# Performance work log

Hardware: AMD Instinct MI355X
Metric: run time of the kernel (lower is better)

## Reference

```python
import jax, jax.numpy as jnp
import numpy as np

B, T, C, H = 4, 2048, 1024, 16
D = C // H  # head_size = 64


def setup_inputs() -> dict:
    key = jax.random.key(0)
    k1, k2, k3 = jax.random.split(key, 3)
    x = jax.random.normal(k1, (B, T, C), dtype=jnp.float32)
    w_qkv = jax.random.normal(k2, (C, 3 * C), dtype=jnp.float32) * (C ** -0.5)
    b_qkv = jnp.zeros((3 * C,), dtype=jnp.float32)
    w_proj = jax.random.normal(k3, (C, C), dtype=jnp.float32) * (C ** -0.5)
    b_proj = jnp.zeros((C,), dtype=jnp.float32)
    return {"x": x, "w_qkv": w_qkv, "b_qkv": b_qkv, "w_proj": w_proj, "b_proj": b_proj}


def reference(x, w_qkv, b_qkv, w_proj, b_proj):
    b, t, c = x.shape
    qkv = x @ w_qkv + b_qkv                      # [B,T,3C]
    q, k, v = jnp.split(qkv, 3, axis=-1)
    # [B,T,C] -> [B,H,T,D]
    q = q.reshape(b, t, H, D).transpose(0, 2, 1, 3)
    k = k.reshape(b, t, H, D).transpose(0, 2, 1, 3)
    v = v.reshape(b, t, H, D).transpose(0, 2, 1, 3)
    attn = jnp.einsum('bhqd,bhkd->bhqk', q, k) * (D ** -0.5)
    causal = jnp.tril(jnp.ones((t, t), dtype=bool))
    attn = jnp.where(causal[None, None], attn, -jnp.inf)
    attn = jax.nn.softmax(attn, axis=-1)
    # dropout: eval mode (identity)
    out = jnp.einsum('bhqk,bhkd->bhqd', attn, v)
    out = out.transpose(0, 2, 1, 3).reshape(b, t, c)
    return out @ w_proj + b_proj
```

## Files before the change

kernel.cpp:

```cpp
#include <hip/hip_runtime.h>

#define B_ 4
#define T_ 2048
#define C_ 1024
#define H_ 16
#define D_ 64

typedef __attribute__((ext_vector_type(8))) short short8;
typedef __attribute__((ext_vector_type(4))) float f32x4;

__device__ inline unsigned short f2bf(float f) {
    union { float f; unsigned u; } v; v.f = f;
    unsigned r = v.u + 0x7fffu + ((v.u >> 16) & 1u);
    return (unsigned short)(r >> 16);
}

__device__ inline unsigned int pk_bf16(float a, float b) {
#if __has_builtin(__builtin_amdgcn_cvt_pk_bf16_f32)
    typedef __attribute__((ext_vector_type(2))) __bf16 bf16x2;
    bf16x2 v = __builtin_amdgcn_cvt_pk_bf16_f32(a, b);
    return __builtin_bit_cast(unsigned int, v);
#else
    return (unsigned)f2bf(a) | ((unsigned)f2bf(b) << 16);
#endif
}

__device__ inline void async_ld16(const void* g, void* lds) {
    __builtin_amdgcn_global_load_lds(
        (const __attribute__((address_space(1))) unsigned int*)g,
        (__attribute__((address_space(3))) unsigned int*)lds, 16, 0, 0);
}

#define MFMA_BF16 __builtin_amdgcn_mfma_f32_16x16x32_bf16

__global__ __launch_bounds__(256) void prep_all(
    const float* __restrict__ x, const float* __restrict__ w_qkv,
    const float* __restrict__ w_proj,
    unsigned short* __restrict__ xb, unsigned short* __restrict__ wqkvT,
    unsigned short* __restrict__ wprojT)
{
    const int bid = blockIdx.x;
    if (bid < 8192) {
        int i = (bid * 256 + threadIdx.x) * 4;
        float4 v = *(const float4*)(x + i);
        uint2 o;
        o.x = pk_bf16(v.x, v.y);
        o.y = pk_bf16(v.z, v.w);
        *(uint2*)(xb + i) = o;
        return;
    }
    __shared__ float tile[32][33];
    const int tt = bid - 8192;
    int bx = tt & 127;
    const int by = tt >> 7;
    const float* src; unsigned short* dst; int Cc;
    if (bx < 96) { src = w_qkv;  dst = wqkvT;  Cc = 3072; }
    else         { src = w_proj; dst = wprojT; Cc = 1024; bx -= 96; }
    const int tx = threadIdx.x & 31, ty = threadIdx.x >> 5;
    #pragma unroll
    for (int r = 0; r < 32; r += 8)
        tile[ty + r][tx] = src[(size_t)(by*32 + ty + r) * Cc + bx*32 + tx];
    __syncthreads();
    #pragma unroll
    for (int r = 0; r < 32; r += 8)
        dst[(size_t)(bx*32 + ty + r) * 1024 + by*32 + tx] = f2bf(tile[tx][ty + r]);
}

__global__ __launch_bounds__(256) void gemm_qkv(
    const unsigned short* __restrict__ A,
    const unsigned short* __restrict__ BT,
    const float* __restrict__ bias,
    unsigned short* __restrict__ qb, unsigned short* __restrict__ kb,
    unsigned short* __restrict__ vtb)
{
    __shared__ unsigned short As[2][128 * 64];
    __shared__ unsigned short Bs[2][128 * 64];
    const int tid = threadIdx.x;
    const int wave = tid >> 6, lane = tid & 63;
    const int wm = wave >> 1, wn = wave & 1;
    const int l15 = lane & 15, lq = lane >> 4;
    const int bid = blockIdx.x;
    const int xcd = bid & 7, idx = bid >> 3;
    const int m0 = (xcd * 8 + (idx & 7)) * 128;
    const int n0 = (idx >> 3) * 128;
    const int sel = n0 >> 10;
    const int row8 = lane >> 3;
    const int chx8 = ((lane & 7) ^ row8) * 8;
    const int cxa = l15 & 7;

    f32x4 acc[4][4] = {};

#define STAGE(buf, K0) do { _Pragma("unroll") \
    for (int c = 0; c < 4; ++c) { \
        const int r = wave*32 + c*8; \
        async_ld16(A  + (size_t)(m0 + r + row8)*1024 + (K0) + chx8, \
                   (char*)&As[buf][0] + r*128); \
        async_ld16(BT + (size_t)(n0 + r + row8)*1024 + (K0) + chx8, \
                   (char*)&Bs[buf][0] + r*128); \
    } } while (0)

    STAGE(0, 0);
    __syncthreads();

    for (int t = 0; t < 16; ++t) {
        const int cur = t & 1;
        if (t < 15) STAGE(cur ^ 1, (t + 1) << 6);
        const unsigned short* Ac = &As[cur][0];
        const unsigned short* Bc = &Bs[cur][0];
        #pragma unroll
        for (int ks = 0; ks < 2; ++ks) {
            short8 af[4], bf[4];
            #pragma unroll
            for (int i = 0; i < 4; ++i) {
                const int ra = wm*64 + i*16 + l15;
                const int rb = wn*64 + i*16 + l15;
                af[i] = *(const short8*)&Ac[ra*64 + (((ks*4 + lq) ^ cxa) << 3)];
                bf[i] = *(const short8*)&Bc[rb*64 + (((ks*4 + lq) ^ cxa) << 3)];
            }
            if (sel < 2) {
                #pragma unroll
                for (int mi = 0; mi < 4; ++mi)
                    #pragma unroll
                    for (int ni = 0; ni < 4; ++ni)
                        acc[mi][ni] = MFMA_BF16(bf[ni], af[mi], acc[mi][ni], 0, 0, 0);
            } else {
                #pragma unroll
                for (int mi = 0; mi < 4; ++mi)
                    #pragma unroll
                    for (int ni = 0; ni < 4; ++ni)
                        acc[mi][ni] = MFMA_BF16(af[mi], bf[ni], acc[mi][ni], 0, 0, 0);
            }
        }
        __syncthreads();
    }
#undef STAGE

    if (sel < 2) {
        const float qs = (sel == 0) ? 0.180336880f : 1.0f;
        unsigned short* dst = (sel == 0) ? qb : kb;
        #pragma unroll
        for (int mi = 0; mi < 4; ++mi) {
            const int t = m0 + wm*64 + mi*16 + l15;
            const int bb = t >> 11, tt = t & 2047;
            #pragma unroll
            for (int ni = 0; ni < 4; ++ni) {
                const int nb = n0 + wn*64 + ni*16 + lq*4;
                const int hh = (nb >> 6) & 15, d0 = nb & 63;
                float4 bv = *(const float4*)(bias + nb);
                float v0 = (acc[mi][ni][0] + bv.x) * qs;
                float v1 = (acc[mi][ni][1] + bv.y) * qs;
                float v2 = (acc[mi][ni][2] + bv.z) * qs;
                float v3 = (acc[mi][ni][3] + bv.w) * qs;
                uint2 pk; pk.x = pk_bf16(v0, v1); pk.y = pk_bf16(v2, v3);
                *(uint2*)(dst + ((size_t)(bb*16 + hh)*2048 + tt)*64 + d0) = pk;
            }
        }
    } else {
        #pragma unroll
        for (int mi = 0; mi < 4; ++mi) {
            const int t0 = m0 + wm*64 + mi*16 + lq*4;
            const int bb = t0 >> 11, tt = t0 & 2047;
            const int tl = tt & 63;
            const int tp = (tt & ~63) | (tl & 32) | ((tl & 12) << 1) | ((tl & 16) >> 2);
            #pragma unroll
            for (int ni = 0; ni < 4; ++ni) {
                const int n = n0 + wn*64 + ni*16 + l15;
                const int hh = (n >> 6) & 15, d = n & 63;
                const float bs = bias[n];
                uint2 pk;
                pk.x = pk_bf16(acc[mi][ni][0] + bs, acc[mi][ni][1] + bs);
                pk.y = pk_bf16(acc[mi][ni][2] + bs, acc[mi][ni][3] + bs);
                *(uint2*)(vtb + ((size_t)(bb*16 + hh)*64 + d)*2048 + tp) = pk;
            }
        }
    }
}

__global__ __launch_bounds__(256) void gemm_proj(
    const unsigned short* __restrict__ A,
    const unsigned short* __restrict__ BT,
    const float* __restrict__ bias,
    float* __restrict__ out)
{
    __shared__ unsigned short As[2][128 * 64];
    __shared__ unsigned short Bs[2][128 * 64];
    const int tid = threadIdx.x;
    const int wave = tid >> 6, lane = tid & 63;
    const int wm = wave >> 1, wn = wave & 1;
    const int l15 = lane & 15, lq = lane >> 4;
    const int bid = blockIdx.x;
    const int xcd = bid & 7, idx = bid >> 3;
    const int m0 = (xcd * 8 + (idx & 7)) * 128;
    const int n0 = (idx >> 3) * 128;
    const int row8 = lane >> 3;
    const int chx8 = ((lane & 7) ^ row8) * 8;
    const int cxa = l15 & 7;

    f32x4 acc[4][4] = {};

#define PSTAGE(buf, K0) do { _Pragma("unroll") \
    for (int c = 0; c < 4; ++c) { \
        const int r = wave*32 + c*8; \
        async_ld16(A  + (size_t)(m0 + r + row8)*1024 + (K0) + chx8, \
                   (char*)&As[buf][0] + r*128); \
        async_ld16(BT + (size_t)(n0 + r + row8)*1024 + (K0) + chx8, \
                   (char*)&Bs[buf][0] + r*128); \
    } } while (0)

    PSTAGE(0, 0);
    __syncthreads();

    for (int t = 0; t < 16; ++t) {
        const int cur = t & 1;
        if (t < 15) PSTAGE(cur ^ 1, (t + 1) << 6);
        const unsigned short* Ac = &As[cur][0];
        const unsigned short* Bc = &Bs[cur][0];
        #pragma unroll
        for (int ks = 0; ks < 2; ++ks) {
            short8 af[4], bf[4];
            #pragma unroll
            for (int i = 0; i < 4; ++i) {
                const int ra = wm*64 + i*16 + l15;
                const int rb = wn*64 + i*16 + l15;
                af[i] = *(const short8*)&Ac[ra*64 + (((ks*4 + lq) ^ cxa) << 3)];
                bf[i] = *(const short8*)&Bc[rb*64 + (((ks*4 + lq) ^ cxa) << 3)];
            }
            #pragma unroll
            for (int mi = 0; mi < 4; ++mi)
                #pragma unroll
                for (int ni = 0; ni < 4; ++ni)
                    acc[mi][ni] = MFMA_BF16(bf[ni], af[mi], acc[mi][ni], 0, 0, 0);
        }
        __syncthreads();
    }
#undef PSTAGE

    #pragma unroll
    for (int mi = 0; mi < 4; ++mi) {
        const int m = m0 + wm*64 + mi*16 + l15;
        #pragma unroll
        for (int ni = 0; ni < 4; ++ni) {
            const int nb = n0 + wn*64 + ni*16 + lq*4;
            float4 bv = *(const float4*)(bias + nb);
            float4 o;
            o.x = acc[mi][ni][0] + bv.x;
            o.y = acc[mi][ni][1] + bv.y;
            o.z = acc[mi][ni][2] + bv.z;
            o.w = acc[mi][ni][3] + bv.w;
            *(float4*)(out + (size_t)m * 1024 + nb) = o;
        }
    }
}

__global__ __launch_bounds__(256, 2) void attn_mfma(
    const unsigned short* __restrict__ qb,
    const unsigned short* __restrict__ kb,
    const unsigned short* __restrict__ vtb,
    unsigned short* __restrict__ ab)
{
    extern __shared__ unsigned char smem[];
    const int tid  = threadIdx.x;
    const int wave = tid >> 6, lane = tid & 63;
    const int l15  = lane & 15, lq = lane >> 4;
    const int linear = blockIdx.x;
    const int xc  = linear & 7;
    const int idx = linear >> 3;
    const int bh  = xc * 8 + (idx & 7);
    const int qblk = 31 - (idx >> 3);
    const int q0 = qblk * 64;
    const int b = bh >> 4, h = bh & 15;
    const size_t base = (size_t)bh * 2048 * 64;

    unsigned short* Kw = (unsigned short*)(smem + wave * 16384);
    unsigned short* Vw = Kw + 4096;

    const int row8 = lane >> 3;
    const int chx8 = ((lane & 7) ^ row8) * 8;

#define STAGE_K(J0) do { _Pragma("unroll") for (int op = 0; op < 8; ++op) \
    async_ld16(kb + base + (size_t)((J0) + op*8 + row8)*64 + chx8, \
               (char*)Kw + op*1024); } while (0)
#define STAGE_V(J0) do { _Pragma("unroll") for (int op = 0; op < 8; ++op) \
    async_ld16(vtb + base + (size_t)(op*8 + row8)*2048 + (J0) + chx8, \
               (char*)Vw + op*1024); } while (0)

    short8 qf[2][4];
    #pragma unroll
    for (int ks = 0; ks < 2; ++ks)
        #pragma unroll
        for (int nq = 0; nq < 4; ++nq)
            qf[ks][nq] = *(const short8*)(qb + base
                + (size_t)(q0 + nq*16 + l15)*64 + ks*32 + lq*8);

    f32x4 o[4][4] = {};
    float lacc[4] = {0.f, 0.f, 0.f, 0.f};

    const int jfirst = wave * 64;
    const int nt = (qblk >= wave) ? ((qblk - wave) >> 2) + 1 : 0;

    if (nt > 0) { STAGE_K(jfirst); STAGE_V(jfirst); }

    for (int i = 0; i < nt; ++i) {
        const int j0 = jfirst + i * 256;
        const bool more = (i + 1 < nt);

        asm volatile("s_waitcnt vmcnt(8)" ::: "memory");

        short8 kf0[4], kf1[4];
        #pragma unroll
        for (int ni = 0; ni < 4; ++ni) {
            const unsigned short* kr = Kw + (ni*16 + l15) * 64;
            kf0[ni] = *(const short8*)(kr + (((0*4 + lq) ^ (l15 & 7)) << 3));
            kf1[ni] = *(const short8*)(kr + (((1*4 + lq) ^ (l15 & 7)) << 3));
        }
        f32x4 s[4][4] = {};
        #pragma unroll
        for (int ni = 0; ni < 4; ++ni)
            #pragma unroll
            for (int nq = 0; nq < 4; ++nq) {
                s[ni][nq] = MFMA_BF16(kf0[ni], qf[0][nq], s[ni][nq], 0, 0, 0);
                s[ni][nq] = MFMA_BF16(kf1[ni], qf[1][nq], s[ni][nq], 0, 0, 0);
            }
        asm volatile("s_waitcnt lgkmcnt(0)" ::: "memory");
        if (more) STAGE_K(j0 + 256);

        if (j0 == q0) {
            #pragma unroll
            for (int ni = 0; ni < 4; ++ni)
                #pragma unroll
                for (int nq = 0; nq < 4; ++nq)
                    #pragma unroll
                    for (int r = 0; r < 4; ++r)
                        if (ni*16 + lq*4 + r > nq*16 + l15)
                            s[ni][nq][r] = -1e30f;
        }

        short8 pf[2][4];
        #pragma unroll
        for (int c = 0; c < 2; ++c)
            #pragma unroll
            for (int nq = 0; nq < 4; ++nq) {
                float p0 = __builtin_amdgcn_exp2f(s[2*c  ][nq][0]);
                float p1 = __builtin_amdgcn_exp2f(s[2*c  ][nq][1]);
                float p2 = __builtin_amdgcn_exp2f(s[2*c  ][nq][2]);
                float p3 = __builtin_amdgcn_exp2f(s[2*c  ][nq][3]);
                float p4 = __builtin_amdgcn_exp2f(s[2*c+1][nq][0]);
                float p5 = __builtin_amdgcn_exp2f(s[2*c+1][nq][1]);
                float p6 = __builtin_amdgcn_exp2f(s[2*c+1][nq][2]);
                float p7 = __builtin_amdgcn_exp2f(s[2*c+1][nq][3]);
                lacc[nq] += ((p0 + p1) + (p2 + p3)) + ((p4 + p5) + (p6 + p7));
                uint4 pu;
                pu.x = pk_bf16(p0, p1); pu.y = pk_bf16(p2, p3);
                pu.z = pk_bf16(p4, p5); pu.w = pk_bf16(p6, p7);
                pf[c][nq] = __builtin_bit_cast(short8, pu);
            }

        if (more) asm volatile("s_waitcnt vmcnt(8)" ::: "memory");
        else      asm volatile("s_waitcnt vmcnt(0)" ::: "memory");

        #pragma unroll
        for (int c = 0; c < 2; ++c) {
            short8 vf[4];
            #pragma unroll
            for (int nd = 0; nd < 4; ++nd)
                vf[nd] = *(const short8*)(Vw + (nd*16 + l15) * 64
                    + (((c*4 + lq) ^ (l15 & 7)) << 3));
            #pragma unroll
            for (int nq = 0; nq < 4; ++nq)
                #pragma unroll
                for (int nd = 0; nd < 4; ++nd)
                    o[nq][nd] = MFMA_BF16(pf[c][nq], vf[nd], o[nq][nd], 0, 0, 0);
        }
        asm volatile("s_waitcnt lgkmcnt(0)" ::: "memory");
        if (more) STAGE_V(j0 + 256);
    }
#undef STAGE_K
#undef STAGE_V

    #pragma unroll
    for (int nq = 0; nq < 4; ++nq) {
        float t = lacc[nq];
        t += __shfl_xor(t, 16);
        t += __shfl_xor(t, 32);
        if (lq == 0) ((float*)Kw)[nq*16 + l15] = t;
    }
    __syncthreads();
    const int qg = wave, d = lane;
    f32x4 linv4[4];
    #pragma unroll
    for (int j = 0; j < 4; ++j) {
        f32x4 lsum = {};
        #pragma unroll
        for (int w2 = 0; w2 < 4; ++w2)
            lsum += *(const f32x4*)((const float*)(smem + w2*16384) + qg*16 + j*4);
        #pragma unroll
        for (int r = 0; r < 4; ++r)
            linv4[j][r] = __builtin_amdgcn_rcpf(lsum[r]);
    }
    __syncthreads();
    #pragma unroll
    for (int nq = 0; nq < 4; ++nq)
        #pragma unroll
        for (int nd = 0; nd < 4; ++nd) {
            const int row = nd*16 + l15;
            const int col = (nq*16 + lq*4 + 4*l15) & 63;
            *(f32x4*)((float*)Kw + row*64 + col) = o[nq][nd];
        }
    __syncthreads();
    #pragma unroll
    for (int j = 0; j < 4; ++j) {
        const int colb = (qg*16 + j*4 + 4*(d & 15)) & 63;
        f32x4 acc = {};
        #pragma unroll
        for (int w2 = 0; w2 < 4; ++w2)
            acc += *(const f32x4*)((const float*)(smem + w2*16384) + d*64 + colb);
        #pragma unroll
        for (int r = 0; r < 4; ++r) {
            const int q = qg*16 + j*4 + r;
            ab[(size_t)(b*2048 + q0 + q)*1024 + h*64 + d] = f2bf(acc[r] * linv4[j][r]);
        }
    }
}

extern "C" void kernel_launch(void* const* d_in, const int* in_sizes, int n_in,
                              void* d_out, int out_size, void* d_ws, size_t ws_size,
                              hipStream_t stream) {
    const float* x      = (const float*)d_in[0];
    const float* w_qkv  = (const float*)d_in[1];
    const float* b_qkv  = (const float*)d_in[2];
    const float* w_proj = (const float*)d_in[3];
    const float* b_proj = (const float*)d_in[4];
    float* out = (float*)d_out;

    unsigned short* xb     = (unsigned short*)d_ws;
    unsigned short* wqkvT  = xb + 8388608;
    unsigned short* wprojT = wqkvT + 3145728;
    unsigned short* qbuf   = wprojT + 1048576;
    unsigned short* kbuf   = qbuf + 8388608;
    unsigned short* vtbuf  = kbuf + 8388608;
    unsigned short* abuf   = vtbuf + 8388608;

    prep_all<<<12288, 256, 0, stream>>>(x, w_qkv, w_proj, xb, wqkvT, wprojT);
    gemm_qkv<<<1536, 256, 0, stream>>>(xb, wqkvT, b_qkv, qbuf, kbuf, vtbuf);
    attn_mfma<<<2048, 256, 65536, stream>>>(qbuf, kbuf, vtbuf, abuf);
    gemm_proj<<<512, 256, 0, stream>>>(abuf, wprojT, b_proj, out);
}
```

Baseline: 237.7 us.

## Halve GEMM K-tile to 32, raise occupancy, and hand-schedule async-load pipeline

Both GEMM kernels (QKV and output projection) now stage 32-wide K slices instead of 64, which halves LDS per block, and request 3 blocks per CU through launch bounds. The loop now uses explicit vmcnt/lgkmcnt waits, raw s_barrier, sched_barrier fences and setprio around the MFMA block, with a new swizzle for the smaller tile. The aim is more resident blocks and better overlap of global loads with MFMA work. In exchange it doubles the number of barriers per K step, and the register cap from the occupancy hint may cause spills.

```diff
diff --git a/kernel.cpp b/kernel.cpp
--- a/kernel.cpp
+++ b/kernel.cpp
@@ -66,15 +66,15 @@
         dst[(size_t)(bx*32 + ty + r) * 1024 + by*32 + tx] = f2bf(tile[tx][ty + r]);
 }
 
-__global__ __launch_bounds__(256) void gemm_qkv(
+__global__ __launch_bounds__(256, 3) void gemm_qkv(
     const unsigned short* __restrict__ A,
     const unsigned short* __restrict__ BT,
     const float* __restrict__ bias,
     unsigned short* __restrict__ qb, unsigned short* __restrict__ kb,
     unsigned short* __restrict__ vtb)
 {
-    __shared__ unsigned short As[2][128 * 64];
-    __shared__ unsigned short Bs[2][128 * 64];
+    __shared__ unsigned short As[2][128 * 32];
+    __shared__ unsigned short Bs[2][128 * 32];
     const int tid = threadIdx.x;
     const int wave = tid >> 6, lane = tid & 63;
     const int wm = wave >> 1, wn = wave & 1;
@@ -84,54 +84,61 @@
     const int m0 = (xcd * 8 + (idx & 7)) * 128;
     const int n0 = (idx >> 3) * 128;
     const int sel = n0 >> 10;
-    const int row8 = lane >> 3;
-    const int chx8 = ((lane & 7) ^ row8) * 8;
-    const int cxa = l15 & 7;
+    const int srow4 = lane >> 2;
+    const int schx  = ((lane & 3) ^ ((lane >> 3) & 3)) * 8;
+    const int rdch = ((lq ^ ((l15 >> 1) & 3)) << 4);
 
     f32x4 acc[4][4] = {};
 
 #define STAGE(buf, K0) do { _Pragma("unroll") \
-    for (int c = 0; c < 4; ++c) { \
-        const int r = wave*32 + c*8; \
-        async_ld16(A  + (size_t)(m0 + r + row8)*1024 + (K0) + chx8, \
-                   (char*)&As[buf][0] + r*128); \
-        async_ld16(BT + (size_t)(n0 + r + row8)*1024 + (K0) + chx8, \
-                   (char*)&Bs[buf][0] + r*128); \
+    for (int c = 0; c < 2; ++c) { \
+        const int R0 = (wave*2 + c) * 16; \
+        async_ld16(A  + (size_t)(m0 + R0 + srow4)*1024 + (K0) + schx, \
+                   (char*)&As[buf][0] + R0*64); \
+        async_ld16(BT + (size_t)(n0 + R0 + srow4)*1024 + (K0) + schx, \
+                   (char*)&Bs[buf][0] + R0*64); \
     } } while (0)
 
     STAGE(0, 0);
-    __syncthreads();
-
-    for (int t = 0; t < 16; ++t) {
+
+    #pragma unroll 2
+    for (int t = 0; t < 32; ++t) {
         const int cur = t & 1;
-        if (t < 15) STAGE(cur ^ 1, (t + 1) << 6);
-        const unsigned short* Ac = &As[cur][0];
-        const unsigned short* Bc = &Bs[cur][0];
-        #pragma unroll
-        for (int ks = 0; ks < 2; ++ks) {
-            short8 af[4], bf[4];
-            #pragma unroll
-            for (int i = 0; i < 4; ++i) {
-                const int ra = wm*64 + i*16 + l15;
-                const int rb = wn*64 + i*16 + l15;
-                af[i] = *(const short8*)&Ac[ra*64 + (((ks*4 + lq) ^ cxa) << 3)];
-                bf[i] = *(const short8*)&Bc[rb*64 + (((ks*4 + lq) ^ cxa) << 3)];
-            }
-            if (sel < 2) {
+        if (t < 31) {
+            STAGE(cur ^ 1, (t + 1) << 5);
+            asm volatile("s_waitcnt vmcnt(4)" ::: "memory");
+        } else {
+            asm volatile("s_waitcnt vmcnt(0)" ::: "memory");
+        }
+        __builtin_amdgcn_s_barrier();
+        __builtin_amdgcn_sched_barrier(0);
+        short8 af[4], bf[4];
+        #pragma unroll
+        for (int i = 0; i < 4; ++i) {
+            af[i] = *(const short8*)((const char*)&As[cur][0]
+                        + (wm*64 + i*16 + l15)*64 + rdch);
+            bf[i] = *(const short8*)((const char*)&Bs[cur][0]
+                        + (wn*64 + i*16 + l15)*64 + rdch);
+        }
+        asm volatile("s_waitcnt lgkmcnt(0)" ::: "memory");
+        __builtin_amdgcn_sched_barrier(0);
+        __builtin_amdgcn_s_setprio(1);
+        if (sel < 2) {
+            #pragma unroll
+            for (int mi = 0; mi < 4; ++mi)
                 #pragma unroll
-                for (int mi = 0; mi < 4; ++mi)
-                    #pragma unroll
-                    for (int ni = 0; ni < 4; ++ni)
-                        acc[mi][ni] = MFMA_BF16(bf[ni], af[mi], acc[mi][ni], 0, 0, 0);
-            } else {
+                for (int ni = 0; ni < 4; ++ni)
+                    acc[mi][ni] = MFMA_BF16(bf[ni], af[mi], acc[mi][ni], 0, 0, 0);
+        } else {
+            #pragma unroll
+            for (int mi = 0; mi < 4; ++mi)
                 #pragma unroll
-                for (int mi = 0; mi < 4; ++mi)
-                    #pragma unroll
-                    for (int ni = 0; ni < 4; ++ni)
-                        acc[mi][ni] = MFMA_BF16(af[mi], bf[ni], acc[mi][ni], 0, 0, 0);
-            }
-        }
-        __syncthreads();
+                for (int ni = 0; ni < 4; ++ni)
+                    acc[mi][ni] = MFMA_BF16(af[mi], bf[ni], acc[mi][ni], 0, 0, 0);
+        }
+        __builtin_amdgcn_s_setprio(0);
+        __builtin_amdgcn_s_barrier();
+        __builtin_amdgcn_sched_barrier(0);
     }
 #undef STAGE
 
@@ -176,14 +183,14 @@
     }
 }
 
-__global__ __launch_bounds__(256) void gemm_proj(
+__global__ __launch_bounds__(256, 3) void gemm_proj(
     const unsigned short* __restrict__ A,
     const unsigned short* __restrict__ BT,
     const float* __restrict__ bias,
     float* __restrict__ out)
 {
-    __shared__ unsigned short As[2][128 * 64];
-    __shared__ unsigned short Bs[2][128 * 64];
+    __shared__ unsigned short As[2][128 * 32];
+    __shared__ unsigned short Bs[2][128 * 32];
     const int tid = threadIdx.x;
     const int wave = tid >> 6, lane = tid & 63;
     const int wm = wave >> 1, wn = wave & 1;
@@ -192,46 +199,53 @@
     const int xcd = bid & 7, idx = bid >> 3;
     const int m0 = (xcd * 8 + (idx & 7)) * 128;
     const int n0 = (idx >> 3) * 128;
-    const int row8 = lane >> 3;
-    const int chx8 = ((lane & 7) ^ row8) * 8;
-    const int cxa = l15 & 7;
+    const int srow4 = lane >> 2;
+    const int schx  = ((lane & 3) ^ ((lane >> 3) & 3)) * 8;
+    const int rdch = ((lq ^ ((l15 >> 1) & 3)) << 4);
 
     f32x4 acc[4][4] = {};
 
 #define PSTAGE(buf, K0) do { _Pragma("unroll") \
-    for (int c = 0; c < 4; ++c) { \
-        const int r = wave*32 + c*8; \
-        async_ld16(A  + (size_t)(m0 + r + row8)*1024 + (K0) + chx8, \
-                   (char*)&As[buf][0] + r*128); \
-        async_ld16(BT + (size_t)(n0 + r + row8)*1024 + (K0) + chx8, \
-                   (char*)&Bs[buf][0] + r*128); \
+    for (int c = 0; c < 2; ++c) { \
+        const int R0 = (wave*2 + c) * 16; \
+        async_ld16(A  + (size_t)(m0 + R0 + srow4)*1024 + (K0) + schx, \
+                   (char*)&As[buf][0] + R0*64); \
+        async_ld16(BT + (size_t)(n0 + R0 + srow4)*1024 + (K0) + schx, \
+                   (char*)&Bs[buf][0] + R0*64); \
     } } while (0)
 
     PSTAGE(0, 0);
-    __syncthreads();
-
-    for (int t = 0; t < 16; ++t) {
+
+    #pragma unroll 2
+    for (int t = 0; t < 32; ++t) {
         const int cur = t & 1;
-        if (t < 15) PSTAGE(cur ^ 1, (t + 1) << 6);
-        const unsigned short* Ac = &As[cur][0];
-        const unsigned short* Bc = &Bs[cur][0];
-        #pragma unroll
-        for (int ks = 0; ks < 2; ++ks) {
-            short8 af[4], bf[4];
-            #pragma unroll
-            for (int i = 0; i < 4; ++i) {
-                const int ra = wm*64 + i*16 + l15;
-                const int rb = wn*64 + i*16 + l15;
-                af[i] = *(const short8*)&Ac[ra*64 + (((ks*4 + lq) ^ cxa) << 3)];
-                bf[i] = *(const short8*)&Bc[rb*64 + (((ks*4 + lq) ^ cxa) << 3)];
-            }
-            #pragma unroll
-            for (int mi = 0; mi < 4; ++mi)
-                #pragma unroll
-                for (int ni = 0; ni < 4; ++ni)
-                    acc[mi][ni] = MFMA_BF16(bf[ni], af[mi], acc[mi][ni], 0, 0, 0);
-        }
-        __syncthreads();
+        if (t < 31) {
+            PSTAGE(cur ^ 1, (t + 1) << 5);
+            asm volatile("s_waitcnt vmcnt(4)" ::: "memory");
+        } else {
+            asm volatile("s_waitcnt vmcnt(0)" ::: "memory");
+        }
+        __builtin_amdgcn_s_barrier();
+        __builtin_amdgcn_sched_barrier(0);
+        short8 af[4], bf[4];
+        #pragma unroll
+        for (int i = 0; i < 4; ++i) {
+            af[i] = *(const short8*)((const char*)&As[cur][0]
+                        + (wm*64 + i*16 + l15)*64 + rdch);
+            bf[i] = *(const short8*)((const char*)&Bs[cur][0]
+                        + (wn*64 + i*16 + l15)*64 + rdch);
+        }
+        asm volatile("s_waitcnt lgkmcnt(0)" ::: "memory");
+        __builtin_amdgcn_sched_barrier(0);
+        __builtin_amdgcn_s_setprio(1);
+        #pragma unroll
+        for (int mi = 0; mi < 4; ++mi)
+            #pragma unroll
+            for (int ni = 0; ni < 4; ++ni)
+                acc[mi][ni] = MFMA_BF16(bf[ni], af[mi], acc[mi][ni], 0, 0, 0);
+        __builtin_amdgcn_s_setprio(0);
+        __builtin_amdgcn_s_barrier();
+        __builtin_amdgcn_sched_barrier(0);
     }
 #undef PSTAGE
 
```

After: 325.6 us. 1.37x slower.

## Enlarge QKV GEMM tile to 256x128 and drop LDS double buffering

Applied to the files above, without the earlier changes.

The QKV projection GEMM now computes a 256x128 output tile per block instead of 128x128, so each wave holds 8x4 accumulator fragments and B-tile data is reused across twice as many rows. The grid is halved to 768 blocks. The double-buffered async prefetch is replaced by a single buffer with load, sync, compute, sync per K step, which keeps the LDS footprint the same but removes the overlap of global loads with MFMA work. Register pressure rises with the doubled accumulator count, which can lower occupancy.

```diff
diff --git a/kernel.cpp b/kernel.cpp
--- a/kernel.cpp
+++ b/kernel.cpp
@@ -73,59 +73,57 @@
     unsigned short* __restrict__ qb, unsigned short* __restrict__ kb,
     unsigned short* __restrict__ vtb)
 {
-    __shared__ unsigned short As[2][128 * 64];
-    __shared__ unsigned short Bs[2][128 * 64];
+    __shared__ unsigned short As[256 * 64];
+    __shared__ unsigned short Bs[128 * 64];
     const int tid = threadIdx.x;
     const int wave = tid >> 6, lane = tid & 63;
     const int wm = wave >> 1, wn = wave & 1;
     const int l15 = lane & 15, lq = lane >> 4;
     const int bid = blockIdx.x;
     const int xcd = bid & 7, idx = bid >> 3;
-    const int m0 = (xcd * 8 + (idx & 7)) * 128;
-    const int n0 = (idx >> 3) * 128;
+    const int m0 = (xcd * 4 + (idx & 3)) * 256;
+    const int n0 = (idx >> 2) * 128;
     const int sel = n0 >> 10;
     const int row8 = lane >> 3;
     const int chx8 = ((lane & 7) ^ row8) * 8;
     const int cxa = l15 & 7;
 
-    f32x4 acc[4][4] = {};
-
-#define STAGE(buf, K0) do { _Pragma("unroll") \
-    for (int c = 0; c < 4; ++c) { \
-        const int r = wave*32 + c*8; \
-        async_ld16(A  + (size_t)(m0 + r + row8)*1024 + (K0) + chx8, \
-                   (char*)&As[buf][0] + r*128); \
-        async_ld16(BT + (size_t)(n0 + r + row8)*1024 + (K0) + chx8, \
-                   (char*)&Bs[buf][0] + r*128); \
-    } } while (0)
-
-    STAGE(0, 0);
-    __syncthreads();
-
-    for (int t = 0; t < 16; ++t) {
-        const int cur = t & 1;
-        if (t < 15) STAGE(cur ^ 1, (t + 1) << 6);
-        const unsigned short* Ac = &As[cur][0];
-        const unsigned short* Bc = &Bs[cur][0];
+    f32x4 acc[8][4] = {};
+
+    for (int k0 = 0; k0 < 1024; k0 += 64) {
+        #pragma unroll
+        for (int c = 0; c < 8; ++c) {
+            const int r = wave*64 + c*8;
+            async_ld16(A + (size_t)(m0 + r + row8)*1024 + k0 + chx8,
+                       (char*)As + r*128);
+        }
+        #pragma unroll
+        for (int c = 0; c < 4; ++c) {
+            const int r = wave*32 + c*8;
+            async_ld16(BT + (size_t)(n0 + r + row8)*1024 + k0 + chx8,
+                       (char*)Bs + r*128);
+        }
+        __syncthreads();
         #pragma unroll
         for (int ks = 0; ks < 2; ++ks) {
-            short8 af[4], bf[4];
-            #pragma unroll
-            for (int i = 0; i < 4; ++i) {
-                const int ra = wm*64 + i*16 + l15;
-                const int rb = wn*64 + i*16 + l15;
-                af[i] = *(const short8*)&Ac[ra*64 + (((ks*4 + lq) ^ cxa) << 3)];
-                bf[i] = *(const short8*)&Bc[rb*64 + (((ks*4 + lq) ^ cxa) << 3)];
-            }
+            short8 af[8], bf[4];
+            #pragma unroll
+            for (int i = 0; i < 8; ++i)
+                af[i] = *(const short8*)&As[(wm*128 + i*16 + l15) * 64
+                                            + (((ks*4 + lq) ^ cxa) << 3)];
+            #pragma unroll
+            for (int j = 0; j < 4; ++j)
+                bf[j] = *(const short8*)&Bs[(wn*64 + j*16 + l15) * 64
+                                            + (((ks*4 + lq) ^ cxa) << 3)];
             if (sel < 2) {
                 #pragma unroll
-                for (int mi = 0; mi < 4; ++mi)
+                for (int mi = 0; mi < 8; ++mi)
                     #pragma unroll
                     for (int ni = 0; ni < 4; ++ni)
                         acc[mi][ni] = MFMA_BF16(bf[ni], af[mi], acc[mi][ni], 0, 0, 0);
             } else {
                 #pragma unroll
-                for (int mi = 0; mi < 4; ++mi)
+                for (int mi = 0; mi < 8; ++mi)
                     #pragma unroll
                     for (int ni = 0; ni < 4; ++ni)
                         acc[mi][ni] = MFMA_BF16(af[mi], bf[ni], acc[mi][ni], 0, 0, 0);
@@ -133,14 +131,13 @@
         }
         __syncthreads();
     }
-#undef STAGE
 
     if (sel < 2) {
         const float qs = (sel == 0) ? 0.180336880f : 1.0f;
         unsigned short* dst = (sel == 0) ? qb : kb;
         #pragma unroll
-        for (int mi = 0; mi < 4; ++mi) {
-            const int t = m0 + wm*64 + mi*16 + l15;
+        for (int mi = 0; mi < 8; ++mi) {
+            const int t = m0 + wm*128 + mi*16 + l15;
             const int bb = t >> 11, tt = t & 2047;
             #pragma unroll
             for (int ni = 0; ni < 4; ++ni) {
@@ -157,8 +154,8 @@
         }
     } else {
         #pragma unroll
-        for (int mi = 0; mi < 4; ++mi) {
-            const int t0 = m0 + wm*64 + mi*16 + lq*4;
+        for (int mi = 0; mi < 8; ++mi) {
+            const int t0 = m0 + wm*128 + mi*16 + lq*4;
             const int bb = t0 >> 11, tt = t0 & 2047;
             const int tl = tt & 63;
             const int tp = (tt & ~63) | (tl & 32) | ((tl & 12) << 1) | ((tl & 16) >> 2);
@@ -441,7 +438,7 @@
     unsigned short* abuf   = vtbuf + 8388608;
 
     prep_all<<<12288, 256, 0, stream>>>(x, w_qkv, w_proj, xb, wqkvT, wprojT);
-    gemm_qkv<<<1536, 256, 0, stream>>>(xb, wqkvT, b_qkv, qbuf, kbuf, vtbuf);
+    gemm_qkv<<<768, 256, 0, stream>>>(xb, wqkvT, b_qkv, qbuf, kbuf, vtbuf);
     attn_mfma<<<2048, 256, 65536, stream>>>(qbuf, kbuf, vtbuf, abuf);
     gemm_proj<<<512, 256, 0, stream>>>(abuf, wprojT, b_proj, out);
 }
```

Result: slower. 260.6 us (+9.6%).

## Replace double-buffered QKV GEMM pipeline with single-stage 128-wide K tiles

Applied to the files above, without the earlier changes.

The QKV projection GEMM no longer prefetches the next K tile while computing the current one. Each iteration now loads a 128-wide K chunk into both shared buffers, synchronizes, and computes on it. This halves the number of loop iterations and barriers, but memory loads no longer overlap with MFMA work, which exposes global load latency.

```diff
diff --git a/kernel.cpp b/kernel.cpp
--- a/kernel.cpp
+++ b/kernel.cpp
@@ -90,32 +90,28 @@
 
     f32x4 acc[4][4] = {};
 
-#define STAGE(buf, K0) do { _Pragma("unroll") \
-    for (int c = 0; c < 4; ++c) { \
-        const int r = wave*32 + c*8; \
-        async_ld16(A  + (size_t)(m0 + r + row8)*1024 + (K0) + chx8, \
-                   (char*)&As[buf][0] + r*128); \
-        async_ld16(BT + (size_t)(n0 + r + row8)*1024 + (K0) + chx8, \
-                   (char*)&Bs[buf][0] + r*128); \
-    } } while (0)
-
-    STAGE(0, 0);
-    __syncthreads();
-
-    for (int t = 0; t < 16; ++t) {
-        const int cur = t & 1;
-        if (t < 15) STAGE(cur ^ 1, (t + 1) << 6);
-        const unsigned short* Ac = &As[cur][0];
-        const unsigned short* Bc = &Bs[cur][0];
-        #pragma unroll
-        for (int ks = 0; ks < 2; ++ks) {
+    for (int k0 = 0; k0 < 1024; k0 += 128) {
+        #pragma unroll
+        for (int s = 0; s < 2; ++s)
+            #pragma unroll
+            for (int c = 0; c < 4; ++c) {
+                const int r = wave*32 + c*8;
+                async_ld16(A  + (size_t)(m0 + r + row8)*1024 + k0 + s*64 + chx8,
+                           (char*)&As[s][0] + r*128);
+                async_ld16(BT + (size_t)(n0 + r + row8)*1024 + k0 + s*64 + chx8,
+                           (char*)&Bs[s][0] + r*128);
+            }
+        __syncthreads();
+        #pragma unroll
+        for (int ks = 0; ks < 4; ++ks) {
+            const int sub = ks >> 1, kk = ks & 1;
             short8 af[4], bf[4];
             #pragma unroll
             for (int i = 0; i < 4; ++i) {
                 const int ra = wm*64 + i*16 + l15;
                 const int rb = wn*64 + i*16 + l15;
-                af[i] = *(const short8*)&Ac[ra*64 + (((ks*4 + lq) ^ cxa) << 3)];
-                bf[i] = *(const short8*)&Bc[rb*64 + (((ks*4 + lq) ^ cxa) << 3)];
+                af[i] = *(const short8*)&As[sub][ra*64 + (((kk*4 + lq) ^ cxa) << 3)];
+                bf[i] = *(const short8*)&Bs[sub][rb*64 + (((kk*4 + lq) ^ cxa) << 3)];
             }
             if (sel < 2) {
                 #pragma unroll
@@ -133,7 +129,6 @@
         }
         __syncthreads();
     }
-#undef STAGE
 
     if (sel < 2) {
         const float qs = (sel == 0) ? 0.180336880f : 1.0f;
```

New measurement: 238.6 us. No clear change (+0.4%).
